# Optimization experiments

Hardware: AMD Instinct MI355X
Metric: run time of the kernel (lower is better)

The kernel has to match this reference:

```python
import jax, jax.numpy as jnp
import numpy as np

N, B, C, H = 4096, 8, 512, 8
D = C // H
EPS = 1e-6


def setup_inputs() -> dict:
    key = jax.random.key(0)
    ks = jax.random.split(key, 6)
    scale = 0.02  # keep projections in a sane range so sigmoid isn't saturated
    return {
        "query": jax.random.normal(ks[0], (N, B, C), dtype=jnp.float32),
        "Wq": jax.random.normal(ks[1], (C, C), dtype=jnp.float32) * scale,
        "bq": jnp.zeros((C,), dtype=jnp.float32),
        "Wk": jax.random.normal(ks[2], (C, C), dtype=jnp.float32) * scale,
        "bk": jnp.zeros((C,), dtype=jnp.float32),
        "Wv": jax.random.normal(ks[3], (C, C), dtype=jnp.float32) * scale,
        "bv": jnp.zeros((C,), dtype=jnp.float32),
        "Wo": jax.random.normal(ks[4], (C, C), dtype=jnp.float32) * scale,
        "bo": jnp.zeros((C,), dtype=jnp.float32),
        "temperature": jnp.ones((1,), dtype=jnp.float32),
    }


def _dot(a, b):
    # a: (B,H,S,D), b: (B,H,D) -> (B,H,S)
    return jnp.einsum("bhsd,bhd->bhs", a, b)


def reference(query, Wq, bq, Wk, bk, Wv, bv, Wo, bo, temperature):
    n, b, c = query.shape  # self-attention: key = value = identity = query
    q = (query @ Wq + bq).reshape(n, b, H, D).transpose(1, 2, 0, 3)  # (B,H,N,D)
    k = (query @ Wk + bk).reshape(n, b, H, D).transpose(1, 2, 0, 3)  # (B,H,HW,D)
    v = (query @ Wv + bv).reshape(n, b, H, D).transpose(1, 2, 0, 3)  # (B,H,HW,D)
    q = jax.nn.sigmoid(q)  # kernel feature map
    k = jax.nn.sigmoid(k)

    hw = k.shape[2]
    # conservation normalizations (note: sum(a+eps, b) adds eps INSIDE the dot, matching torch)
    sink_incoming = 1.0 / (_dot(q + EPS, k.sum(axis=2) + EPS) + EPS)        # (B,H,N)
    source_outgoing = 1.0 / (_dot(k + EPS, q.sum(axis=2) + EPS) + EPS)      # (B,H,HW)
    conserved_sink = _dot(q + EPS, (k * source_outgoing[..., None]).sum(axis=2) + EPS) + EPS
    conserved_source = _dot(k + EPS, (q * sink_incoming[..., None]).sum(axis=2) + EPS) + EPS
    conserved_source = jnp.clip(conserved_source, -1.0, 1.0)

    sink_allocation = jax.nn.sigmoid(conserved_sink * (float(n) / float(hw)))  # (B,H,N)
    # torch does softmax over the key axis and multiplies by key.shape[2] == embed_dim C
    source_competition = jax.nn.softmax(conserved_source / temperature, axis=-1) * float(c)  # (B,H,HW)

    kv = jnp.einsum("bhsd,bhse->bhde", k, v * source_competition[..., None])  # (B,H,D,D)
    out_update = jnp.einsum("bhnd,bhde->bhne", q, kv)
    out_update = out_update * sink_incoming[..., None] * sink_allocation[..., None]  # (B,H,N,D)

    # faithful to torch: reshape (B,H,N,D) -> (B,N,C) directly (no head permute)
    out = out_update.reshape(b, n, c)
    out = out @ Wo + bo
    out = out.transpose(1, 0, 2)  # back to (N,B,C)
    return query + out  # identity residual (dropout is identity in eval)
```

## Files before the change

### kernel.cpp

```cpp
#include <hip/hip_runtime.h>
#include <stdint.h>

typedef unsigned short u16;
typedef unsigned int u32;

#define EPS 1e-6f
#define NSEQ 4096

typedef __bf16 bf16x8 __attribute__((ext_vector_type(8)));
typedef float f32x4 __attribute__((ext_vector_type(4)));

__device__ __forceinline__ float b2f(u16 u) {
  union { u32 i; float f; } x; x.i = ((u32)u) << 16; return x.f;
}
__device__ __forceinline__ u16 f2b(float f) {
  union { float f; u32 i; } x; x.f = f;
  u32 r = x.i + 0x7fffu + ((x.i >> 16) & 1u);
  return (u16)(r >> 16);
}
__device__ __forceinline__ u16 f2b_hw(float f) {
  union { __bf16 h; u16 u; } x; x.h = (__bf16)f; return x.u;
}
__device__ __forceinline__ void unpack8(const u16* p, float* o) {
  uint4 u = *(const uint4*)p;
  o[0]=b2f((u16)(u.x&0xffff)); o[1]=b2f((u16)(u.x>>16));
  o[2]=b2f((u16)(u.y&0xffff)); o[3]=b2f((u16)(u.y>>16));
  o[4]=b2f((u16)(u.z&0xffff)); o[5]=b2f((u16)(u.z>>16));
  o[6]=b2f((u16)(u.w&0xffff)); o[7]=b2f((u16)(u.w>>16));
}
__device__ __forceinline__ bool is_f32(const u16* tdisc) { return tdisc[0] != 0x3F80; }

__global__ void convert_small(const void* bq, const void* bk, const void* bv,
                              const void* bo, const void* temp,
                              float* __restrict__ bcat, float* __restrict__ scal) {
  bool f32 = is_f32((const u16*)temp);
  int t = threadIdx.x;
  for (int i = t; i < 512; i += 256) {
    bcat[i]      = f32 ? ((const float*)bq)[i] : b2f(((const u16*)bq)[i]);
    bcat[512+i]  = f32 ? ((const float*)bk)[i] : b2f(((const u16*)bk)[i]);
    bcat[1024+i] = f32 ? ((const float*)bv)[i] : b2f(((const u16*)bv)[i]);
    bcat[1536+i] = f32 ? ((const float*)bo)[i] : b2f(((const u16*)bo)[i]);
  }
  if (t == 0) scal[0] = f32 ? ((const float*)temp)[0] : b2f(((const u16*)temp)[0]);
}

__global__ void zero_small(float* __restrict__ qsum, float* __restrict__ ksum,
                           float* __restrict__ qsi, float* __restrict__ kso) {
  int i = blockIdx.x*256 + threadIdx.x;
  qsum[i]=0.f; ksum[i]=0.f; qsi[i]=0.f; kso[i]=0.f;
}

__global__ __launch_bounds__(256) void conv_q(const void* __restrict__ query,
                                              u16* __restrict__ Qbf,
                                              const u16* __restrict__ tdisc) {
  bool f32 = is_f32(tdisc);
  int i = (blockIdx.x*256 + threadIdx.x) * 8;
  if (f32) {
    const float* q = (const float*)query + i;
    float4 a = ((const float4*)q)[0];
    float4 b = ((const float4*)q)[1];
    union { u16 h[8]; uint4 u; } pk;
    pk.h[0]=f2b_hw(a.x); pk.h[1]=f2b_hw(a.y); pk.h[2]=f2b_hw(a.z); pk.h[3]=f2b_hw(a.w);
    pk.h[4]=f2b_hw(b.x); pk.h[5]=f2b_hw(b.y); pk.h[6]=f2b_hw(b.z); pk.h[7]=f2b_hw(b.w);
    *(uint4*)(Qbf + i) = pk.u;
  } else {
    *(uint4*)(Qbf + i) = *(const uint4*)((const u16*)query + i);
  }
}

__global__ void transpose_w(const void* Wq, const void* Wk,
                            const void* Wv, const void* Wo,
                            u16* __restrict__ Wt, const void* temp) {
  __shared__ u16 tile[32][33];
  bool f32 = is_f32((const u16*)temp);
  int wsel = blockIdx.z;
  const void* W = wsel==0?Wq:wsel==1?Wk:wsel==2?Wv:Wo;
  int x0 = blockIdx.x*32, y0 = blockIdx.y*32;
  int tx = threadIdx.x & 31, ty = threadIdx.x >> 5;
  #pragma unroll
  for (int i=0;i<32;i+=8) {
    int idx = (y0+ty+i)*512 + x0+tx;
    tile[ty+i][tx] = f32 ? f2b(((const float*)W)[idx]) : ((const u16*)W)[idx];
  }
  __syncthreads();
  #pragma unroll
  for (int i=0;i<32;i+=8)
    Wt[wsel*262144 + (x0+ty+i)*512 + (y0+tx)] = tile[tx][ty+i];
}

template<int MODE, bool GLOADA>
__global__ __launch_bounds__(256, 3) void gemm_kernel(
    const void* __restrict__ A, const u16* __restrict__ WtAll,
    const float* __restrict__ bcat, const void* __restrict__ query,
    u16* __restrict__ Qb, u16* __restrict__ Kb, u16* __restrict__ Vb,
    void* __restrict__ Outp, float* __restrict__ qsum, float* __restrict__ ksum,
    const u16* __restrict__ tdisc)
{
  __shared__ __align__(16) u16 smem[MODE==0 ? 17408 : 16384];
  bool f32 = is_f32(tdisc);
  int t = threadIdx.x;
  int lane = t & 63, w = t >> 6;
  int wr = w >> 1, wc = w & 1;
  int quad = lane >> 4, l15 = lane & 15;
  int orig = blockIdx.x;
  int wgid, y, bx;
  if (MODE==0) {
    wgid = (orig & 7) * 384 + (orig >> 3);
    y = wgid % 12; bx = wgid / 12;
  } else {
    wgid = (orig & 7) * 128 + (orig >> 3);
    y = wgid & 3;  bx = wgid >> 2;
  }
  int row0 = bx * 128;
  int wsel = (MODE==0) ? (y >> 2) : 3;
  int colw = (MODE==0) ? ((y & 3)*128) : (y*128);
  const u16* Bt = WtAll + wsel*262144 + colw*512;
  const u16* Abf = (const u16*)A;

  f32x4 zero4 = {0.f, 0.f, 0.f, 0.f};
  f32x4 acc[4][4];
  #pragma unroll
  for (int i=0;i<4;i++)
    #pragma unroll
    for (int j=0;j<4;j++) acc[i][j] = zero4;

  int sr = t >> 1;
  int scol = (t & 1) * 16;
  int aoff0 = sr*32 + scol;
  int aoff1 = sr*32 + scol + 8;
  int grow = t >> 2;
  int gcol = (t & 3) * 8;
  bool af32 = (MODE==0) && f32;

  float4 x0, x1, x2, x3;
  uint4 u0, u1;

  if (GLOADA) {
    __builtin_amdgcn_global_load_lds(
        (const __attribute__((address_space(1))) void*)(Abf + (size_t)(row0 + grow)*512 + gcol),
        (__attribute__((address_space(3))) void*)(smem + t*8), 16, 0, 0);
    __builtin_amdgcn_global_load_lds(
        (const __attribute__((address_space(1))) void*)(Abf + (size_t)(row0 + 64 + grow)*512 + gcol),
        (__attribute__((address_space(3))) void*)(smem + 2048 + t*8), 16, 0, 0);
  } else {
    if (af32) {
      const float* Af = (const float*)A + (row0+sr)*512 + scol;
      x0 = ((const float4*)Af)[0]; x1 = ((const float4*)Af)[1];
      x2 = ((const float4*)Af)[2]; x3 = ((const float4*)Af)[3];
    } else {
      const u16* Au = (const u16*)A + (row0+sr)*512 + scol;
      u0 = *(const uint4*)Au; u1 = *(const uint4*)(Au + 8);
    }
  }
  __builtin_amdgcn_global_load_lds(
      (const __attribute__((address_space(1))) void*)(Bt + (grow     )*512 + gcol),
      (__attribute__((address_space(3))) void*)(smem + 4096 + t*8), 16, 0, 0);
  __builtin_amdgcn_global_load_lds(
      (const __attribute__((address_space(1))) void*)(Bt + (grow + 64)*512 + gcol),
      (__attribute__((address_space(3))) void*)(smem + 4096 + 2048 + t*8), 16, 0, 0);
  if (!GLOADA) {
    union { u16 h[16]; uint4 u[2]; } ab;
    if (af32) {
      ab.h[0]=f2b_hw(x0.x);  ab.h[1]=f2b_hw(x0.y);  ab.h[2]=f2b_hw(x0.z);  ab.h[3]=f2b_hw(x0.w);
      ab.h[4]=f2b_hw(x1.x);  ab.h[5]=f2b_hw(x1.y);  ab.h[6]=f2b_hw(x1.z);  ab.h[7]=f2b_hw(x1.w);
      ab.h[8]=f2b_hw(x2.x);  ab.h[9]=f2b_hw(x2.y);  ab.h[10]=f2b_hw(x2.z); ab.h[11]=f2b_hw(x2.w);
      ab.h[12]=f2b_hw(x3.x); ab.h[13]=f2b_hw(x3.y); ab.h[14]=f2b_hw(x3.z); ab.h[15]=f2b_hw(x3.w);
    } else { ab.u[0] = u0; ab.u[1] = u1; }
    *(uint4*)(smem + aoff0) = ab.u[0];
    *(uint4*)(smem + aoff1) = ab.u[1];
  }
  __syncthreads();

  for (int tt = 0; tt < 16; ++tt) {
    const u16* bc = smem + ((tt & 1) ? 8192 : 0);
    u16* bn = smem + ((tt & 1) ? 0 : 8192);
    bool more = tt < 15;
    int k1 = (tt + 1) * 32;
    if (more) {
      if (GLOADA) {
        __builtin_amdgcn_global_load_lds(
            (const __attribute__((address_space(1))) void*)(Abf + (size_t)(row0 + grow)*512 + k1 + gcol),
            (__attribute__((address_space(3))) void*)(bn + t*8), 16, 0, 0);
        __builtin_amdgcn_global_load_lds(
            (const __attribute__((address_space(1))) void*)(Abf + (size_t)(row0 + 64 + grow)*512 + k1 + gcol),
            (__attribute__((address_space(3))) void*)(bn + 2048 + t*8), 16, 0, 0);
      } else {
        if (af32) {
          const float* Af = (const float*)A + (row0+sr)*512 + k1 + scol;
          x0 = ((const float4*)Af)[0]; x1 = ((const float4*)Af)[1];
          x2 = ((const float4*)Af)[2]; x3 = ((const float4*)Af)[3];
        } else {
          const u16* Au = (const u16*)A + (row0+sr)*512 + k1 + scol;
          u0 = *(const uint4*)Au; u1 = *(const uint4*)(Au + 8);
        }
      }
      __builtin_amdgcn_global_load_lds(
          (const __attribute__((address_space(1))) void*)(Bt + (grow     )*512 + k1 + gcol),
          (__attribute__((address_space(3))) void*)(bn + 4096 + t*8), 16, 0, 0);
      __builtin_amdgcn_global_load_lds(
          (const __attribute__((address_space(1))) void*)(Bt + (grow + 64)*512 + k1 + gcol),
          (__attribute__((address_space(3))) void*)(bn + 4096 + 2048 + t*8), 16, 0, 0);
    }
    bf16x8 af[4], bfr[4];
    #pragma unroll
    for (int mt=0;mt<4;mt++)
      af[mt] = *(const bf16x8*)(bc + (wr*64 + mt*16 + l15)*32 + quad*8);
    #pragma unroll
    for (int nt=0;nt<4;nt++)
      bfr[nt] = *(const bf16x8*)(bc + 4096 + (wc*64 + nt*16 + l15)*32 + quad*8);
    #pragma unroll
    for (int mt=0;mt<4;mt++)
      #pragma unroll
      for (int nt=0;nt<4;nt++)
        acc[mt][nt] = __builtin_amdgcn_mfma_f32_16x16x32_bf16(af[mt], bfr[nt], acc[mt][nt], 0, 0, 0);
    if (more) {
      if (!GLOADA) {
        union { u16 h[16]; uint4 u[2]; } ab;
        if (af32) {
          ab.h[0]=f2b_hw(x0.x);  ab.h[1]=f2b_hw(x0.y);  ab.h[2]=f2b_hw(x0.z);  ab.h[3]=f2b_hw(x0.w);
          ab.h[4]=f2b_hw(x1.x);  ab.h[5]=f2b_hw(x1.y);  ab.h[6]=f2b_hw(x1.z);  ab.h[7]=f2b_hw(x1.w);
          ab.h[8]=f2b_hw(x2.x);  ab.h[9]=f2b_hw(x2.y);  ab.h[10]=f2b_hw(x2.z); ab.h[11]=f2b_hw(x2.w);
          ab.h[12]=f2b_hw(x3.x); ab.h[13]=f2b_hw(x3.y); ab.h[14]=f2b_hw(x3.z); ab.h[15]=f2b_hw(x3.w);
        } else { ab.u[0] = u0; ab.u[1] = u1; }
        *(uint4*)(bn + aoff0) = ab.u[0];
        *(uint4*)(bn + aoff1) = ab.u[1];
      }
      __syncthreads();
    }
  }

  const float* bias = bcat + wsel*512;
  if (MODE==0) {
    u16* Cs = smem;
    __syncthreads();
    #pragma unroll
    for (int mt=0;mt<4;mt++) {
      #pragma unroll
      for (int nt=0;nt<4;nt++) {
        #pragma unroll
        for (int pp=0;pp<4;pp++) {
          int m = wr*64 + mt*16 + quad*4 + pp;
          int c = wc*64 + nt*16 + l15;
          float val = acc[mt][nt][pp] + bias[colw + c];
          if (wsel < 2) val = 1.f/(1.f+__expf(-val));
          Cs[m*136 + c] = f2b_hw(val);
        }
      }
    }
    __syncthreads();
    u16* dst = wsel==0?Qb:wsel==1?Kb:Vb;
    #pragma unroll
    for (int i=0;i<8;i++) {
      int idx = i*256 + t;
      int d8 = idx & 7, hl = (idx>>3)&1, m = idx>>4;
      int r = row0 + m;
      int bi = r & 7, nrow = r >> 3;
      int h = (colw >> 6) + hl;
      uint4 v = *(const uint4*)(Cs + m*136 + hl*64 + d8*8);
      *(uint4*)(dst + (((size_t)(bi*8+h))*NSEQ + nrow)*64 + d8*8) = v;
    }
    if (wsel < 2) {
      float* outp = wsel==0 ? qsum : ksum;
      #pragma unroll
      for (int i=0;i<4;i++) {
        int idx = i*256 + t;
        int c = idx & 127, bi = idx >> 7;
        float s = 0.f;
        #pragma unroll
        for (int j=0;j<16;j++) s += b2f(Cs[(j*8+bi)*136 + c]);
        int jj = colw + c; int h = jj>>6, d = jj&63;
        atomicAdd(&outp[(bi*8+h)*64 + d], s);
      }
    }
  } else {
    float* Cf = (float*)smem;
    const float* q32 = (const float*)query;
    const u16*  q16 = (const u16*)query;
    #pragma unroll
    for (int half=0; half<2; half++) {
      __syncthreads();
      if (wr == half) {
        #pragma unroll
        for (int mt=0;mt<4;mt++) {
          #pragma unroll
          for (int nt=0;nt<4;nt++) {
            #pragma unroll
            for (int pp=0;pp<4;pp++) {
              int m = mt*16 + quad*4 + pp;
              int cl = wc*64 + nt*16 + l15;
              Cf[m*128 + cl] = acc[mt][nt][pp] + bias[colw + cl];
            }
          }
        }
      }
      __syncthreads();
      #pragma unroll
      for (int i=0;i<8;i++) {
        int idx = i*256 + t;
        int m = idx >> 5, c4 = (idx & 31)*4;
        int off = (row0 + half*64 + m)*512 + colw + c4;
        float4 v = *(const float4*)&Cf[m*128 + c4];
        if (f32) {
          float4 res = *(const float4*)&q32[off];
          v.x += res.x; v.y += res.y; v.z += res.z; v.w += res.w;
          *(float4*)&((float*)Outp)[off] = v;
        } else {
          union { u16 h[4]; uint2 u; } o;
          o.h[0] = f2b(v.x + b2f(q16[off+0]));
          o.h[1] = f2b(v.y + b2f(q16[off+1]));
          o.h[2] = f2b(v.z + b2f(q16[off+2]));
          o.h[3] = f2b(v.w + b2f(q16[off+3]));
          *(uint2*)&((u16*)Outp)[off] = o.u;
        }
      }
    }
  }
}

__global__ __launch_bounds__(256) void rdcs_kernel(
    const u16* __restrict__ Q, const u16* __restrict__ K,
    const float* __restrict__ qsum, const float* __restrict__ ksum,
    float* __restrict__ si, float* __restrict__ so,
    float* __restrict__ qsi, float* __restrict__ kso) {
  int p = blockIdx.x & 63, chunk = blockIdx.x >> 6;
  int t = threadIdx.x, part = t & 7, rsub = t >> 3;
  float ks_e[8], qs_e[8];
  #pragma unroll
  for (int j=0;j<8;j++) {
    ks_e[j] = ksum[p*64 + part*8 + j] + EPS;
    qs_e[j] = qsum[p*64 + part*8 + j] + EPS;
  }
  float qacc[8] = {0,0,0,0,0,0,0,0}, kacc[8] = {0,0,0,0,0,0,0,0};
  #pragma unroll
  for (int g=0; g<4; ++g) {
    int r = chunk*128 + g*32 + rsub;
    float fq[8], fk[8];
    unpack8(Q + ((size_t)p*NSEQ + r)*64 + part*8, fq);
    unpack8(K + ((size_t)p*NSEQ + r)*64 + part*8, fk);
    float a1 = 0.f, a2 = 0.f;
    #pragma unroll
    for (int j=0;j<8;j++) { a1 += (fq[j]+EPS)*ks_e[j]; a2 += (fk[j]+EPS)*qs_e[j]; }
    #pragma unroll
    for (int s=1; s<8; s<<=1) { a1 += __shfl_xor(a1, s, 8); a2 += __shfl_xor(a2, s, 8); }
    float siv = 1.f/(a1+EPS), sov = 1.f/(a2+EPS);
    if (part == 0) { si[p*NSEQ+r] = siv; so[p*NSEQ+r] = sov; }
    #pragma unroll
    for (int j=0;j<8;j++) { qacc[j] += fq[j]*siv; kacc[j] += fk[j]*sov; }
  }
  __shared__ float red[32][64];
  #pragma unroll
  for (int j=0;j<8;j++) red[rsub][part*8+j] = qacc[j];
  __syncthreads();
  if (t < 64) {
    float s = 0.f;
    #pragma unroll
    for (int g=0;g<32;g++) s += red[g][t];
    atomicAdd(&qsi[p*64+t], s);
  }
  __syncthreads();
  #pragma unroll
  for (int j=0;j<8;j++) red[rsub][part*8+j] = kacc[j];
  __syncthreads();
  if (t < 64) {
    float s = 0.f;
    #pragma unroll
    for (int g=0;g<32;g++) s += red[g][t];
    atomicAdd(&kso[p*64+t], s);
  }
}

__global__ __launch_bounds__(256) void rowdot_kernel(const u16* __restrict__ Q, const u16* __restrict__ K,
                              const float* __restrict__ qvec, const float* __restrict__ kvec,
                              float* __restrict__ out1, float* __restrict__ out2) {
  int p = blockIdx.x & 63, chunk = blockIdx.x >> 6;
  int t = threadIdx.x;
  int part = t & 7, rsub = t >> 3;
  int r = chunk*32 + rsub;
  float kv_e[8], qv_e[8];
  #pragma unroll
  for (int j=0;j<8;j++) {
    kv_e[j] = kvec[p*64 + part*8 + j] + EPS;
    qv_e[j] = qvec[p*64 + part*8 + j] + EPS;
  }
  float f[8];
  float a1 = 0.f, a2 = 0.f;
  unpack8(Q + ((size_t)p*NSEQ + r)*64 + part*8, f);
  #pragma unroll
  for (int j=0;j<8;j++) a1 += (f[j]+EPS)*kv_e[j];
  unpack8(K + ((size_t)p*NSEQ + r)*64 + part*8, f);
  #pragma unroll
  for (int j=0;j<8;j++) a2 += (f[j]+EPS)*qv_e[j];
  #pragma unroll
  for (int s=4; s>0; s>>=1) {
    a1 += __shfl_down(a1, s, 8);
    a2 += __shfl_down(a2, s, 8);
  }
  if (part == 0) {
    a1 += EPS; a2 += EPS;
    out1[p*NSEQ+r] = 1.f/(1.f+__expf(-a1));
    out2[p*NSEQ+r] = fminf(fmaxf(a2, -1.f), 1.f);
  }
}

__global__ void softmax_kernel(const float* __restrict__ cs, float* __restrict__ sc,
                               float* __restrict__ kvbuf, const float* __restrict__ scal) {
  int p = blockIdx.x, t = threadIdx.x;
  for (int i = t; i < 4096; i += 256) kvbuf[p*4096 + i] = 0.f;
  float invT = 1.f / scal[0];
  float v[16];
  float m = -1e30f;
  #pragma unroll
  for (int i=0;i<16;i++) { v[i] = cs[p*NSEQ + i*256 + t] * invT; m = fmaxf(m, v[i]); }
  __shared__ float red[256];
  red[t] = m; __syncthreads();
  for (int sd=128; sd>0; sd>>=1) { if (t<sd) red[t]=fmaxf(red[t],red[t+sd]); __syncthreads(); }
  m = red[0]; __syncthreads();
  float s = 0.f;
  #pragma unroll
  for (int i=0;i<16;i++) { v[i] = __expf(v[i]-m); s += v[i]; }
  red[t] = s; __syncthreads();
  for (int sd=128; sd>0; sd>>=1) { if (t<sd) red[t]+=red[t+sd]; __syncthreads(); }
  float inv = 512.f / red[0];
  #pragma unroll
  for (int i=0;i<16;i++) sc[p*NSEQ + i*256 + t] = v[i]*inv;
}

__global__ __launch_bounds__(256) void kv_kernel(const u16* __restrict__ K, const u16* __restrict__ V,
                                                 const float* __restrict__ sc, float* __restrict__ kvbuf) {
  int p = blockIdx.x >> 4, chunk = blockIdx.x & 15;
  int t = threadIdx.x;
  int lane = t & 63, w = t >> 6;
  int quad = lane >> 4, l15 = lane & 15;
  __shared__ __align__(16) u16 ks[256*64];
  __shared__ __align__(16) u16 vs[256*64];
  const u16* Kp = K + ((size_t)p*NSEQ + chunk*256)*64;
  const u16* Vp = V + ((size_t)p*NSEQ + chunk*256)*64;
  const float* scp = sc + p*NSEQ + chunk*256;
  #pragma unroll
  for (int i=0;i<8;i++) {
    int l8 = i*256 + t;
    int eoff = l8*8;
    __builtin_amdgcn_global_load_lds(
        (const __attribute__((address_space(1))) void*)(Kp + eoff),
        (__attribute__((address_space(3))) void*)(ks + eoff), 16, 0, 0);
    float f[8]; unpack8(Vp + eoff, f);
    float wgt = scp[l8 >> 3];
    union { u16 h[8]; uint4 u; } pk;
    #pragma unroll
    for (int j=0;j<8;j++) pk.h[j] = f2b(f[j]*wgt);
    *(uint4*)&vs[eoff] = pk.u;
  }
  __syncthreads();
  int wr = w >> 1, wc = w & 1;
  f32x4 zero4 = {0.f,0.f,0.f,0.f};
  f32x4 acc[2][2];
  acc[0][0]=zero4; acc[0][1]=zero4; acc[1][0]=zero4; acc[1][1]=zero4;
  for (int ksb = 0; ksb < 8; ++ksb) {
    int s0 = ksb*32 + quad*8;
    bf16x8 a[2], b[2];
    #pragma unroll
    for (int dt=0; dt<2; ++dt) {
      int d = wr*32 + dt*16 + l15;
      union { u16 h[8]; bf16x8 v; } fa;
      #pragma unroll
      for (int j=0;j<8;j++) fa.h[j] = ks[(s0+j)*64 + d];
      a[dt] = fa.v;
    }
    #pragma unroll
    for (int et=0; et<2; ++et) {
      int e = wc*32 + et*16 + l15;
      union { u16 h[8]; bf16x8 v; } fb;
      #pragma unroll
      for (int j=0;j<8;j++) fb.h[j] = vs[(s0+j)*64 + e];
      b[et] = fb.v;
    }
    #pragma unroll
    for (int dt=0;dt<2;dt++)
      #pragma unroll
      for (int et=0;et<2;et++)
        acc[dt][et] = __builtin_amdgcn_mfma_f32_16x16x32_bf16(a[dt], b[et], acc[dt][et], 0, 0, 0);
  }
  float* kvp = kvbuf + p*4096;
  #pragma unroll
  for (int dt=0;dt<2;dt++)
    #pragma unroll
    for (int et=0;et<2;et++)
      #pragma unroll
      for (int pp=0;pp<4;pp++) {
        int d = wr*32 + dt*16 + quad*4 + pp;
        int e = wc*32 + et*16 + l15;
        atomicAdd(&kvp[d*64 + e], acc[dt][et][pp]);
      }
}

__global__ __launch_bounds__(256, 3) void outupd_kernel(const u16* __restrict__ Q, const float* __restrict__ kvbuf,
                                                        const float* __restrict__ si, const float* __restrict__ sa,
                                                        u16* __restrict__ OU) {
  __shared__ __align__(16) u16 arena[16384];
  __shared__ float sisa[256];
  int p = blockIdx.x >> 4, chunk = blockIdx.x & 15;
  int t = threadIdx.x;
  int lane = t & 63, w = t >> 6;
  int quad = lane >> 4, l15 = lane & 15;
  int rbase = chunk*256;
  const float* kvp = kvbuf + p*4096;

  {
    int e = t & 63, dg = t >> 6;
    float v[16];
    #pragma unroll
    for (int j=0;j<16;j++) v[j] = kvp[(dg*16+j)*64 + e];
    #pragma unroll
    for (int sl=0; sl<2; sl++) {
      int s = dg*2 + sl;
      union { u16 h[8]; uint4 u; } pk;
      #pragma unroll
      for (int j=0;j<8;j++) pk.h[j] = f2b_hw(v[sl*8+j]);
      *(uint4*)&arena[e*64 + ((s ^ (e&7))<<3)] = pk.u;
    }
    int gr = p*NSEQ + rbase + t;
    sisa[t] = si[gr] * sa[gr];
  }
  __syncthreads();

  bf16x8 bfr[4][2];
  #pragma unroll
  for (int nt=0;nt<4;nt++) {
    int e = nt*16 + l15;
    #pragma unroll
    for (int kk=0;kk<2;kk++)
      bfr[nt][kk] = *(const bf16x8*)&arena[e*64 + (((kk*4+quad) ^ (e&7))<<3)];
  }

  f32x4 zero4 = {0.f,0.f,0.f,0.f};
  f32x4 acc[4][4];
  #pragma unroll
  for (int i=0;i<4;i++)
    #pragma unroll
    for (int j=0;j<4;j++) acc[i][j] = zero4;

  const u16* Qw = Q + ((size_t)(p*NSEQ + rbase + w*64))*64;
  #pragma unroll
  for (int mt=0;mt<4;mt++) {
    const u16* qa = Qw + (mt*16 + l15)*64;
    bf16x8 a0 = *(const bf16x8*)(qa + quad*8);
    bf16x8 a1 = *(const bf16x8*)(qa + 32 + quad*8);
    #pragma unroll
    for (int nt=0;nt<4;nt++) {
      acc[mt][nt] = __builtin_amdgcn_mfma_f32_16x16x32_bf16(a0, bfr[nt][0], acc[mt][nt], 0, 0, 0);
      acc[mt][nt] = __builtin_amdgcn_mfma_f32_16x16x32_bf16(a1, bfr[nt][1], acc[mt][nt], 0, 0, 0);
    }
  }

  __syncthreads();
  #pragma unroll
  for (int mt=0;mt<4;mt++) {
    #pragma unroll
    for (int nt=0;nt<4;nt++) {
      #pragma unroll
      for (int pp=0;pp<4;pp++) {
        int rl = w*64 + mt*16 + quad*4 + pp;
        arena[rl*64 + nt*16 + l15] = f2b_hw(acc[mt][nt][pp] * sisa[rl]);
      }
    }
  }
  __syncthreads();
  u16* dst = OU + ((size_t)(p*NSEQ + rbase + t))*64;
  #pragma unroll
  for (int i=0;i<8;i++) {
    int s = (i + t) & 7;
    *(uint4*)(dst + s*8) = *(const uint4*)&arena[t*64 + s*8];
  }
}

extern "C" void kernel_launch(void* const* d_in, const int* in_sizes, int n_in,
                              void* d_out, int out_size, void* d_ws, size_t ws_size,
                              hipStream_t stream) {
  const void* query = d_in[0];
  const void* Wq = d_in[1];
  const void* bq = d_in[2];
  const void* Wk = d_in[3];
  const void* bk = d_in[4];
  const void* Wv = d_in[5];
  const void* bv = d_in[6];
  const void* Wo = d_in[7];
  const void* bo = d_in[8];
  const void* temp = d_in[9];
  const u16* tdisc = (const u16*)temp;

  char* ws = (char*)d_ws;
  u16*   Vb   = (u16*)(ws + 0);
  u16*   OU   = Vb;
  u16*   Wt   = (u16*)(ws + 33554432);
  float* bcat = (float*)(ws + 35651584);
  float* scal = (float*)(ws + 35659776);
  float* qsum = (float*)(ws + 35667968);
  float* ksum = (float*)(ws + 35684352);
  float* qsi  = (float*)(ws + 35700736);
  float* kso  = (float*)(ws + 35717120);
  float* si   = (float*)(ws + 36700160);
  float* so   = (float*)(ws + 37748736);
  float* sa   = (float*)(ws + 38797312);
  float* cs   = (float*)(ws + 39845888);
  float* sc   = (float*)(ws + 40894464);
  float* kvb  = (float*)(ws + 41943040);
  u16*   Qbf  = (u16*)(ws + 44040192);
  bool bigws = ws_size >= (size_t)44040192 + 33554432;

  u16* Qb = (u16*)d_out;
  u16* Kb = (u16*)d_out + 16777216;

  convert_small<<<1, 256, 0, stream>>>(bq, bk, bv, bo, temp, bcat, scal);
  zero_small<<<16, 256, 0, stream>>>(qsum, ksum, qsi, kso);
  transpose_w<<<dim3(16,16,4), 256, 0, stream>>>(Wq, Wk, Wv, Wo, Wt, temp);
  if (bigws) {
    conv_q<<<8192, 256, 0, stream>>>(query, Qbf, tdisc);
    gemm_kernel<0, true><<<3072, 256, 0, stream>>>(Qbf, Wt, bcat, query,
                                                   Qb, Kb, Vb, nullptr, qsum, ksum, tdisc);
  } else {
    gemm_kernel<0, false><<<3072, 256, 0, stream>>>(query, Wt, bcat, query,
                                                    Qb, Kb, Vb, nullptr, qsum, ksum, tdisc);
  }
  rdcs_kernel<<<2048, 256, 0, stream>>>(Qb, Kb, qsum, ksum, si, so, qsi, kso);
  rowdot_kernel<<<8192, 256, 0, stream>>>(Qb, Kb, qsi, kso, sa, cs);
  softmax_kernel<<<64, 256, 0, stream>>>(cs, sc, kvb, scal);
  kv_kernel<<<1024, 256, 0, stream>>>(Kb, Vb, sc, kvb);
  outupd_kernel<<<1024, 256, 0, stream>>>(Qb, kvb, si, sa, OU);
  gemm_kernel<1, true><<<1024, 256, 0, stream>>>(OU, Wt, bcat, query,
                                                 nullptr, nullptr, nullptr, d_out,
                                                 qsum, ksum, tdisc);
}
```

Before: 313.9 us.

## Triple-buffer GEMM LDS staging, batch rowdot rows per thread, hardware bf16 convert

When A is loaded straight into LDS, the GEMM now uses a three-stage LDS ring. Loads run two k-steps ahead, and waits are tracked with explicit vmcnt counts and s_barrier instead of __syncthreads. The rowdot kernel now handles four rows per thread with all loads issued up front, so its grid shrinks by four. The kv kernel swaps the software bf16 rounding for the hardware conversion. Shared memory grows to 48KB per GEMM block, which may limit occupancy, and the hand-written waitcnt logic is fragile.

```diff
diff --git a/kernel.cpp b/kernel.cpp
--- a/kernel.cpp
+++ b/kernel.cpp
@@ -23,6 +23,12 @@
 }
 __device__ __forceinline__ void unpack8(const u16* p, float* o) {
   uint4 u = *(const uint4*)p;
+  o[0]=b2f((u16)(u.x&0xffff)); o[1]=b2f((u16)(u.x>>16));
+  o[2]=b2f((u16)(u.y&0xffff)); o[3]=b2f((u16)(u.y>>16));
+  o[4]=b2f((u16)(u.z&0xffff)); o[5]=b2f((u16)(u.z>>16));
+  o[6]=b2f((u16)(u.w&0xffff)); o[7]=b2f((u16)(u.w>>16));
+}
+__device__ __forceinline__ void unpack8v(uint4 u, float* o) {
   o[0]=b2f((u16)(u.x&0xffff)); o[1]=b2f((u16)(u.x>>16));
   o[2]=b2f((u16)(u.y&0xffff)); o[3]=b2f((u16)(u.y>>16));
   o[4]=b2f((u16)(u.z&0xffff)); o[5]=b2f((u16)(u.z>>16));
@@ -96,7 +102,7 @@
     void* __restrict__ Outp, float* __restrict__ qsum, float* __restrict__ ksum,
     const u16* __restrict__ tdisc)
 {
-  __shared__ __align__(16) u16 smem[MODE==0 ? 17408 : 16384];
+  __shared__ __align__(16) u16 smem[24576];
   bool f32 = is_f32(tdisc);
   int t = threadIdx.x;
   int lane = t & 63, w = t >> 6;
@@ -132,17 +138,53 @@
   int gcol = (t & 3) * 8;
   bool af32 = (MODE==0) && f32;
 
-  float4 x0, x1, x2, x3;
-  uint4 u0, u1;
-
   if (GLOADA) {
-    __builtin_amdgcn_global_load_lds(
-        (const __attribute__((address_space(1))) void*)(Abf + (size_t)(row0 + grow)*512 + gcol),
-        (__attribute__((address_space(3))) void*)(smem + t*8), 16, 0, 0);
-    __builtin_amdgcn_global_load_lds(
-        (const __attribute__((address_space(1))) void*)(Abf + (size_t)(row0 + 64 + grow)*512 + gcol),
-        (__attribute__((address_space(3))) void*)(smem + 2048 + t*8), 16, 0, 0);
+    auto stage = [&](int boff, int k0) {
+      __builtin_amdgcn_global_load_lds(
+          (const __attribute__((address_space(1))) void*)(Abf + (size_t)(row0 + grow)*512 + k0 + gcol),
+          (__attribute__((address_space(3))) void*)(smem + boff + t*8), 16, 0, 0);
+      __builtin_amdgcn_global_load_lds(
+          (const __attribute__((address_space(1))) void*)(Abf + (size_t)(row0 + 64 + grow)*512 + k0 + gcol),
+          (__attribute__((address_space(3))) void*)(smem + boff + 2048 + t*8), 16, 0, 0);
+      __builtin_amdgcn_global_load_lds(
+          (const __attribute__((address_space(1))) void*)(Bt + (grow     )*512 + k0 + gcol),
+          (__attribute__((address_space(3))) void*)(smem + boff + 4096 + t*8), 16, 0, 0);
+      __builtin_amdgcn_global_load_lds(
+          (const __attribute__((address_space(1))) void*)(Bt + (grow + 64)*512 + k0 + gcol),
+          (__attribute__((address_space(3))) void*)(smem + boff + 4096 + 2048 + t*8), 16, 0, 0);
+    };
+    stage(0, 0);
+    stage(8192, 32);
+    asm volatile("s_waitcnt vmcnt(4)");
+    __builtin_amdgcn_s_barrier();
+
+    int cur = 0;
+    for (int tt = 0; tt < 16; ++tt) {
+      const u16* bc = smem + cur*8192;
+      int nxt2 = (cur == 0) ? 2 : cur - 1;
+      if (tt <= 13) stage(nxt2*8192, (tt + 2) * 32);
+      bf16x8 af[4], bfr[4];
+      #pragma unroll
+      for (int mt=0;mt<4;mt++)
+        af[mt] = *(const bf16x8*)(bc + (wr*64 + mt*16 + l15)*32 + quad*8);
+      #pragma unroll
+      for (int nt=0;nt<4;nt++)
+        bfr[nt] = *(const bf16x8*)(bc + 4096 + (wc*64 + nt*16 + l15)*32 + quad*8);
+      #pragma unroll
+      for (int mt=0;mt<4;mt++)
+        #pragma unroll
+        for (int nt=0;nt<4;nt++)
+          acc[mt][nt] = __builtin_amdgcn_mfma_f32_16x16x32_bf16(af[mt], bfr[nt], acc[mt][nt], 0, 0, 0);
+      if (tt < 15) {
+        if (tt <= 13) asm volatile("s_waitcnt vmcnt(4)" ::: "memory");
+        else          asm volatile("s_waitcnt vmcnt(0)" ::: "memory");
+        __builtin_amdgcn_s_barrier();
+      }
+      cur = (cur == 2) ? 0 : cur + 1;
+    }
   } else {
+    float4 x0, x1, x2, x3;
+    uint4 u0, u1;
     if (af32) {
       const float* Af = (const float*)A + (row0+sr)*512 + scol;
       x0 = ((const float4*)Af)[0]; x1 = ((const float4*)Af)[1];
@@ -151,40 +193,30 @@
       const u16* Au = (const u16*)A + (row0+sr)*512 + scol;
       u0 = *(const uint4*)Au; u1 = *(const uint4*)(Au + 8);
     }
-  }
-  __builtin_amdgcn_global_load_lds(
-      (const __attribute__((address_space(1))) void*)(Bt + (grow     )*512 + gcol),
-      (__attribute__((address_space(3))) void*)(smem + 4096 + t*8), 16, 0, 0);
-  __builtin_amdgcn_global_load_lds(
-      (const __attribute__((address_space(1))) void*)(Bt + (grow + 64)*512 + gcol),
-      (__attribute__((address_space(3))) void*)(smem + 4096 + 2048 + t*8), 16, 0, 0);
-  if (!GLOADA) {
-    union { u16 h[16]; uint4 u[2]; } ab;
-    if (af32) {
-      ab.h[0]=f2b_hw(x0.x);  ab.h[1]=f2b_hw(x0.y);  ab.h[2]=f2b_hw(x0.z);  ab.h[3]=f2b_hw(x0.w);
-      ab.h[4]=f2b_hw(x1.x);  ab.h[5]=f2b_hw(x1.y);  ab.h[6]=f2b_hw(x1.z);  ab.h[7]=f2b_hw(x1.w);
-      ab.h[8]=f2b_hw(x2.x);  ab.h[9]=f2b_hw(x2.y);  ab.h[10]=f2b_hw(x2.z); ab.h[11]=f2b_hw(x2.w);
-      ab.h[12]=f2b_hw(x3.x); ab.h[13]=f2b_hw(x3.y); ab.h[14]=f2b_hw(x3.z); ab.h[15]=f2b_hw(x3.w);
-    } else { ab.u[0] = u0; ab.u[1] = u1; }
-    *(uint4*)(smem + aoff0) = ab.u[0];
-    *(uint4*)(smem + aoff1) = ab.u[1];
-  }
-  __syncthreads();
-
-  for (int tt = 0; tt < 16; ++tt) {
-    const u16* bc = smem + ((tt & 1) ? 8192 : 0);
-    u16* bn = smem + ((tt & 1) ? 0 : 8192);
-    bool more = tt < 15;
-    int k1 = (tt + 1) * 32;
-    if (more) {
-      if (GLOADA) {
-        __builtin_amdgcn_global_load_lds(
-            (const __attribute__((address_space(1))) void*)(Abf + (size_t)(row0 + grow)*512 + k1 + gcol),
-            (__attribute__((address_space(3))) void*)(bn + t*8), 16, 0, 0);
-        __builtin_amdgcn_global_load_lds(
-            (const __attribute__((address_space(1))) void*)(Abf + (size_t)(row0 + 64 + grow)*512 + k1 + gcol),
-            (__attribute__((address_space(3))) void*)(bn + 2048 + t*8), 16, 0, 0);
-      } else {
+    __builtin_amdgcn_global_load_lds(
+        (const __attribute__((address_space(1))) void*)(Bt + (grow     )*512 + gcol),
+        (__attribute__((address_space(3))) void*)(smem + 4096 + t*8), 16, 0, 0);
+    __builtin_amdgcn_global_load_lds(
+        (const __attribute__((address_space(1))) void*)(Bt + (grow + 64)*512 + gcol),
+        (__attribute__((address_space(3))) void*)(smem + 4096 + 2048 + t*8), 16, 0, 0);
+    {
+      union { u16 h[16]; uint4 u[2]; } ab;
+      if (af32) {
+        ab.h[0]=f2b_hw(x0.x);  ab.h[1]=f2b_hw(x0.y);  ab.h[2]=f2b_hw(x0.z);  ab.h[3]=f2b_hw(x0.w);
+        ab.h[4]=f2b_hw(x1.x);  ab.h[5]=f2b_hw(x1.y);  ab.h[6]=f2b_hw(x1.z);  ab.h[7]=f2b_hw(x1.w);
+        ab.h[8]=f2b_hw(x2.x);  ab.h[9]=f2b_hw(x2.y);  ab.h[10]=f2b_hw(x2.z); ab.h[11]=f2b_hw(x2.w);
+        ab.h[12]=f2b_hw(x3.x); ab.h[13]=f2b_hw(x3.y); ab.h[14]=f2b_hw(x3.z); ab.h[15]=f2b_hw(x3.w);
+      } else { ab.u[0] = u0; ab.u[1] = u1; }
+      *(uint4*)(smem + aoff0) = ab.u[0];
+      *(uint4*)(smem + aoff1) = ab.u[1];
+    }
+    __syncthreads();
+    for (int tt = 0; tt < 16; ++tt) {
+      const u16* bc = smem + ((tt & 1) ? 8192 : 0);
+      u16* bn = smem + ((tt & 1) ? 0 : 8192);
+      bool more = tt < 15;
+      int k1 = (tt + 1) * 32;
+      if (more) {
         if (af32) {
           const float* Af = (const float*)A + (row0+sr)*512 + k1 + scol;
           x0 = ((const float4*)Af)[0]; x1 = ((const float4*)Af)[1];
@@ -193,28 +225,26 @@
           const u16* Au = (const u16*)A + (row0+sr)*512 + k1 + scol;
           u0 = *(const uint4*)Au; u1 = *(const uint4*)(Au + 8);
         }
-      }
-      __builtin_amdgcn_global_load_lds(
-          (const __attribute__((address_space(1))) void*)(Bt + (grow     )*512 + k1 + gcol),
-          (__attribute__((address_space(3))) void*)(bn + 4096 + t*8), 16, 0, 0);
-      __builtin_amdgcn_global_load_lds(
-          (const __attribute__((address_space(1))) void*)(Bt + (grow + 64)*512 + k1 + gcol),
-          (__attribute__((address_space(3))) void*)(bn + 4096 + 2048 + t*8), 16, 0, 0);
-    }
-    bf16x8 af[4], bfr[4];
-    #pragma unroll
-    for (int mt=0;mt<4;mt++)
-      af[mt] = *(const bf16x8*)(bc + (wr*64 + mt*16 + l15)*32 + quad*8);
-    #pragma unroll
-    for (int nt=0;nt<4;nt++)
-      bfr[nt] = *(const bf16x8*)(bc + 4096 + (wc*64 + nt*16 + l15)*32 + quad*8);
-    #pragma unroll
-    for (int mt=0;mt<4;mt++)
+        __builtin_amdgcn_global_load_lds(
+            (const __attribute__((address_space(1))) void*)(Bt + (grow     )*512 + k1 + gcol),
+            (__attribute__((address_space(3))) void*)(bn + 4096 + t*8), 16, 0, 0);
+        __builtin_amdgcn_global_load_lds(
+            (const __attribute__((address_space(1))) void*)(Bt + (grow + 64)*512 + k1 + gcol),
+            (__attribute__((address_space(3))) void*)(bn + 4096 + 2048 + t*8), 16, 0, 0);
+      }
+      bf16x8 af[4], bfr[4];
+      #pragma unroll
+      for (int mt=0;mt<4;mt++)
+        af[mt] = *(const bf16x8*)(bc + (wr*64 + mt*16 + l15)*32 + quad*8);
       #pragma unroll
       for (int nt=0;nt<4;nt++)
-        acc[mt][nt] = __builtin_amdgcn_mfma_f32_16x16x32_bf16(af[mt], bfr[nt], acc[mt][nt], 0, 0, 0);
-    if (more) {
-      if (!GLOADA) {
+        bfr[nt] = *(const bf16x8*)(bc + 4096 + (wc*64 + nt*16 + l15)*32 + quad*8);
+      #pragma unroll
+      for (int mt=0;mt<4;mt++)
+        #pragma unroll
+        for (int nt=0;nt<4;nt++)
+          acc[mt][nt] = __builtin_amdgcn_mfma_f32_16x16x32_bf16(af[mt], bfr[nt], acc[mt][nt], 0, 0, 0);
+      if (more) {
         union { u16 h[16]; uint4 u[2]; } ab;
         if (af32) {
           ab.h[0]=f2b_hw(x0.x);  ab.h[1]=f2b_hw(x0.y);  ab.h[2]=f2b_hw(x0.z);  ab.h[3]=f2b_hw(x0.w);
@@ -224,8 +254,8 @@
         } else { ab.u[0] = u0; ab.u[1] = u1; }
         *(uint4*)(bn + aoff0) = ab.u[0];
         *(uint4*)(bn + aoff1) = ab.u[1];
-      }
-      __syncthreads();
+        __syncthreads();
+      }
     }
   }
 
@@ -375,30 +405,40 @@
   int p = blockIdx.x & 63, chunk = blockIdx.x >> 6;
   int t = threadIdx.x;
   int part = t & 7, rsub = t >> 3;
-  int r = chunk*32 + rsub;
   float kv_e[8], qv_e[8];
   #pragma unroll
   for (int j=0;j<8;j++) {
     kv_e[j] = kvec[p*64 + part*8 + j] + EPS;
     qv_e[j] = qvec[p*64 + part*8 + j] + EPS;
   }
-  float f[8];
-  float a1 = 0.f, a2 = 0.f;
-  unpack8(Q + ((size_t)p*NSEQ + r)*64 + part*8, f);
-  #pragma unroll
-  for (int j=0;j<8;j++) a1 += (f[j]+EPS)*kv_e[j];
-  unpack8(K + ((size_t)p*NSEQ + r)*64 + part*8, f);
-  #pragma unroll
-  for (int j=0;j<8;j++) a2 += (f[j]+EPS)*qv_e[j];
-  #pragma unroll
-  for (int s=4; s>0; s>>=1) {
-    a1 += __shfl_down(a1, s, 8);
-    a2 += __shfl_down(a2, s, 8);
-  }
-  if (part == 0) {
-    a1 += EPS; a2 += EPS;
-    out1[p*NSEQ+r] = 1.f/(1.f+__expf(-a1));
-    out2[p*NSEQ+r] = fminf(fmaxf(a2, -1.f), 1.f);
+  uint4 qr[4], kr[4];
+  #pragma unroll
+  for (int g=0; g<4; ++g) {
+    int r = chunk*128 + g*32 + rsub;
+    qr[g] = *(const uint4*)(Q + ((size_t)p*NSEQ + r)*64 + part*8);
+    kr[g] = *(const uint4*)(K + ((size_t)p*NSEQ + r)*64 + part*8);
+  }
+  #pragma unroll
+  for (int g=0; g<4; ++g) {
+    int r = chunk*128 + g*32 + rsub;
+    float f[8];
+    float a1 = 0.f, a2 = 0.f;
+    unpack8v(qr[g], f);
+    #pragma unroll
+    for (int j=0;j<8;j++) a1 += (f[j]+EPS)*kv_e[j];
+    unpack8v(kr[g], f);
+    #pragma unroll
+    for (int j=0;j<8;j++) a2 += (f[j]+EPS)*qv_e[j];
+    #pragma unroll
+    for (int s=4; s>0; s>>=1) {
+      a1 += __shfl_down(a1, s, 8);
+      a2 += __shfl_down(a2, s, 8);
+    }
+    if (part == 0) {
+      a1 += EPS; a2 += EPS;
+      out1[p*NSEQ+r] = 1.f/(1.f+__expf(-a1));
+      out2[p*NSEQ+r] = fminf(fmaxf(a2, -1.f), 1.f);
+    }
   }
 }
 
@@ -447,7 +487,7 @@
     float wgt = scp[l8 >> 3];
     union { u16 h[8]; uint4 u; } pk;
     #pragma unroll
-    for (int j=0;j<8;j++) pk.h[j] = f2b(f[j]*wgt);
+    for (int j=0;j<8;j++) pk.h[j] = f2b_hw(f[j]*wgt);
     *(uint4*)&vs[eoff] = pk.u;
   }
   __syncthreads();
@@ -622,7 +662,7 @@
                                                     Qb, Kb, Vb, nullptr, qsum, ksum, tdisc);
   }
   rdcs_kernel<<<2048, 256, 0, stream>>>(Qb, Kb, qsum, ksum, si, so, qsi, kso);
-  rowdot_kernel<<<8192, 256, 0, stream>>>(Qb, Kb, qsi, kso, sa, cs);
+  rowdot_kernel<<<2048, 256, 0, stream>>>(Qb, Kb, qsi, kso, sa, cs);
   softmax_kernel<<<64, 256, 0, stream>>>(cs, sc, kvb, scal);
   kv_kernel<<<1024, 256, 0, stream>>>(Kb, Vb, sc, kvb);
   outupd_kernel<<<1024, 256, 0, stream>>>(Qb, kvb, si, sa, OU);
```

Result: no change. 319.8 us (+1.9%).
